# Kernel tuning notes

Measured on AMD Instinct MI355X. Metric: run time of the kernel, lower is better.

Reference implementation:

```python
import jax, jax.numpy as jnp
import numpy as np
from jax import lax

N_FEAT = 150          # feature-map side
N_AR = 9              # anchors per cell
PRE_NMS = 6000        # mode='test'
POST_NMS = 300        # mode='test'
IOU_TH = 0.7
MIN_SIZE = 16.0 / 1000.0


def _make_anchors():
    # grid of centers in [0,1], 9 anchors per cell (3 scales x 3 ratios), xyxy form
    cs = (np.arange(N_FEAT) + 0.5) / N_FEAT
    cy, cx = np.meshgrid(cs, cs, indexing='ij')
    scales = np.array([0.05, 0.1, 0.2])
    ratios = np.array([0.5, 1.0, 2.0])
    ws = (scales[:, None] * np.sqrt(ratios)[None, :]).reshape(-1)  # [9]
    hs = (scales[:, None] / np.sqrt(ratios)[None, :]).reshape(-1)
    cx = np.repeat(cx.reshape(-1), N_AR)
    cy = np.repeat(cy.reshape(-1), N_AR)
    ws = np.tile(ws, N_FEAT * N_FEAT)
    hs = np.tile(hs, N_FEAT * N_FEAT)
    xy = np.stack([cx - ws / 2, cy - hs / 2, cx + ws / 2, cy + hs / 2], axis=-1)
    return xy.astype(np.float32)  # [N,4]


def xy_to_cxcy(xy):
    return jnp.concatenate([(xy[:, 2:] + xy[:, :2]) / 2, xy[:, 2:] - xy[:, :2]], axis=-1)


def cxcy_to_xy(cxcy):
    return jnp.concatenate([cxcy[:, :2] - cxcy[:, 2:] / 2, cxcy[:, :2] + cxcy[:, 2:] / 2], axis=-1)


def decode(t, priors_cxcy):
    cxcy = t[:, :2] * priors_cxcy[:, 2:] + priors_cxcy[:, :2]
    wh = jnp.exp(t[:, 2:]) * priors_cxcy[:, 2:]
    return jnp.concatenate([cxcy, wh], axis=-1)


def pairwise_iou(b):
    # b: [K,4] xyxy -> [K,K]
    area = (b[:, 2] - b[:, 0]) * (b[:, 3] - b[:, 1])
    lt = jnp.maximum(b[:, None, :2], b[None, :, :2])
    rb = jnp.minimum(b[:, None, 2:], b[None, :, 2:])
    wh = jnp.clip(rb - lt, 0.0)
    inter = wh[..., 0] * wh[..., 1]
    return inter / (area[:, None] + area[None, :] - inter + 1e-12)


def greedy_nms_mask(boxes, valid):
    # boxes sorted by score desc; returns bool keep mask of shape [K]
    K = boxes.shape[0]
    iou = pairwise_iou(boxes)  # [K,K]  (~144 MB for K=6000)
    idx = jnp.arange(K)

    def body(i, keep):
        active = keep[i] & valid[i]
        supp = (iou[i] > IOU_TH) & (idx > i) & active
        return keep & ~supp

    keep = lax.fori_loop(0, K, body, jnp.ones(K, dtype=bool))
    return keep & valid


def setup_inputs() -> dict:
    key = jax.random.key(0)
    k1, k2 = jax.random.split(key)
    N = N_FEAT * N_FEAT * N_AR
    pred_cls = jax.random.normal(k1, (1, N, 2), dtype=jnp.float32)
    pred_loc = jax.random.normal(k2, (1, N, 4), dtype=jnp.float32) * 0.1
    anchor = jnp.asarray(_make_anchors())
    return {"pred_cls": pred_cls, "pred_loc": pred_loc, "anchor": anchor}


def reference(pred_cls, pred_loc, anchor):
    # squeeze batch dim of 1
    scores = jax.nn.softmax(pred_cls[0], axis=-1)[:, 1]  # [N] objectness
    priors = xy_to_cxcy(anchor)
    roi = jnp.clip(cxcy_to_xy(decode(pred_loc[0], priors)), 0.0, 1.0)  # [N,4]

    ws = roi[:, 2] - roi[:, 0]
    hs = roi[:, 3] - roi[:, 1]
    valid = (ws >= MIN_SIZE) & (hs >= MIN_SIZE)

    # size filter via masking (scores in [0,1], so -1 sorts below all valid)
    scores_m = jnp.where(valid, scores, -1.0)
    top_scores, top_idx = lax.top_k(scores_m, PRE_NMS)
    boxes = roi[top_idx]           # [PRE_NMS,4], score-descending
    valid_k = top_scores >= 0.0

    keep = greedy_nms_mask(boxes, valid_k)  # [PRE_NMS] bool

    # gather kept boxes in score order, take first POST_NMS, zero-pad the rest
    order = jnp.argsort(jnp.where(keep, jnp.arange(PRE_NMS), PRE_NMS))
    sel = order[:POST_NMS]
    out = boxes[sel] * keep[sel][:, None].astype(boxes.dtype)  # [POST_NMS,4]
    return out
```

## Files before the change

### kernel.cpp

```cpp
#include <hip/hip_runtime.h>
#include <hip/hip_bf16.h>

#define NANCH 202500
#define PRE_NMS 6000
#define POST_NMS 300
#define KW 94
#define CAP 8192
#define NBUCK 16384
#define BSHIFT 18
#define IOU_TH 0.7f
#define MIN_SIZE 0.016f
#define TB_PAD 6016
#define RTILE 256
#define RITEMS 8
#define SBLK 256

typedef unsigned long long ull;

__device__ inline float4 decode_box(const float* __restrict__ loc,
                                    const float* __restrict__ anc, int i) {
    float4 a = ((const float4*)anc)[i];
    float4 t = ((const float4*)loc)[i];
    float pw = a.z - a.x, ph = a.w - a.y;
    float pcx = (a.x + a.z) * 0.5f, pcy = (a.y + a.w) * 0.5f;
    float cx = t.x * pw + pcx, cy = t.y * ph + pcy;
    float w = expf(t.z) * pw, h = expf(t.w) * ph;
    float x1 = fminf(fmaxf(cx - 0.5f * w, 0.f), 1.f);
    float y1 = fminf(fmaxf(cy - 0.5f * h, 0.f), 1.f);
    float x2 = fminf(fmaxf(cx + 0.5f * w, 0.f), 1.f);
    float y2 = fminf(fmaxf(cy + 0.5f * h, 0.f), 1.f);
    return make_float4(x1, y1, x2, y2);
}

__device__ inline unsigned make_key(const float* __restrict__ cls,
                                    const float* __restrict__ loc,
                                    const float* __restrict__ anc, int i) {
    float2 c = ((const float2*)cls)[i];
    float d = c.y - c.x;
    float4 b = decode_box(loc, anc, i);
    bool valid = ((b.z - b.x) >= MIN_SIZE) && ((b.w - b.y) >= MIN_SIZE);
    unsigned ib = __float_as_uint(d);
    unsigned u = (ib & 0x80000000u) ? ~ib : (ib | 0x80000000u);
    return valid ? u : 0u;
}

__device__ inline ull orx64(ull v, int m) {
    unsigned lo = (unsigned)v, hi = (unsigned)(v >> 32);
    lo = (unsigned)__shfl_xor((int)lo, m, 64);
    hi = (unsigned)__shfl_xor((int)hi, m, 64);
    return ((ull)hi << 32) | lo;
}

__global__ __launch_bounds__(256) void k_score(const float* __restrict__ cls,
                                               const float* __restrict__ loc,
                                               const float* __restrict__ anc,
                                               unsigned* __restrict__ hist,
                                               unsigned* __restrict__ keyc, int n) {
    __shared__ unsigned lh[NBUCK];
    int tid = threadIdx.x, bid = blockIdx.x;
    for (int q = tid; q < NBUCK; q += 256) lh[q] = 0u;
    __syncthreads();
    for (int i = bid * 256 + tid; i < n; i += SBLK * 256) {
        unsigned u = make_key(cls, loc, anc, i);
        if (keyc) keyc[i] = u;
        atomicAdd(&lh[u >> BSHIFT], 1u);
    }
    __syncthreads();
    for (int qq = 0; qq < NBUCK / 256; qq++) {
        int q = (qq + bid) & (NBUCK / 256 - 1);
        int b = q * 256 + tid;
        unsigned v = lh[b];
        if (v) atomicAdd(&hist[b], v);
    }
}

__global__ __launch_bounds__(1024) void k_findb(const unsigned* __restrict__ hist,
                                                unsigned* __restrict__ meta) {
    __shared__ unsigned ps[1024];
    int t = threadIdx.x;
    int base = t * (NBUCK / 1024);
    unsigned local = 0;
    for (int b = 0; b < NBUCK / 1024; b++) local += hist[base + b];
    ps[t] = local;
    __syncthreads();
    for (int off = 1; off < 1024; off <<= 1) {
        unsigned add = (t + off < 1024) ? ps[t + off] : 0u;
        __syncthreads();
        ps[t] += add;
        __syncthreads();
    }
    unsigned incl = ps[t];
    unsigned excl = incl - local;
    if (incl >= (unsigned)PRE_NMS && excl < (unsigned)PRE_NMS) {
        unsigned cum = excl;
        int B = base;
        for (int b = NBUCK / 1024 - 1; b >= 0; b--) {
            cum += hist[base + b];
            if (cum >= (unsigned)PRE_NMS) { B = base + b; break; }
        }
        meta[0] = (unsigned)B;
    }
}

__global__ __launch_bounds__(256) void k_compactC(const unsigned* __restrict__ keyc,
                                                  unsigned* __restrict__ meta,
                                                  ull* __restrict__ cand, int n) {
    int i = blockIdx.x * blockDim.x + threadIdx.x;
    unsigned u = (i < n) ? keyc[i] : 0u;
    unsigned B = meta[0];
    bool pred = (i < n) && ((u >> BSHIFT) >= B);
    ull mask = __ballot(pred);
    if (!mask) return;
    int lane = threadIdx.x & 63;
    int leader = __builtin_ctzll(mask);
    unsigned base = 0;
    if (lane == leader) base = atomicAdd(&meta[1], (unsigned)__popcll(mask));
    base = (unsigned)__shfl((int)base, leader, 64);
    if (pred) {
        unsigned p = base + (unsigned)__popcll(mask & ((1ull << lane) - 1ull));
        if (p < CAP) cand[p] = ((ull)(~u) << 32) | (unsigned)i;
    }
}

__global__ __launch_bounds__(256) void k_compactR(const float* __restrict__ cls,
                                                  const float* __restrict__ loc,
                                                  const float* __restrict__ anc,
                                                  unsigned* __restrict__ meta,
                                                  ull* __restrict__ cand, int n) {
    int i = blockIdx.x * blockDim.x + threadIdx.x;
    if (i >= n) return;
    unsigned u = make_key(cls, loc, anc, i);
    if ((u >> BSHIFT) >= meta[0]) {
        unsigned p = atomicAdd(&meta[1], 1u);
        if (p < CAP) cand[p] = ((ull)(~u) << 32) | (unsigned)i;
    }
}

__global__ __launch_bounds__(256) void k_rank(const ull* __restrict__ cand,
                                              const unsigned* __restrict__ meta,
                                              unsigned* __restrict__ rank,
                                              float4* __restrict__ topbox) {
    __shared__ __align__(16) ull tile[RTILE];
    int tid = threadIdx.x;
    int bx = blockIdx.x, by = blockIdx.y;
    unsigned C = meta[1]; if (C > CAP) C = CAP;
    if (by == 0) {
        int per = TB_PAD / (CAP / (256 * RITEMS));
        int s0 = bx * per;
        for (int q = tid; q < per; q += 256)
            topbox[s0 + q] = make_float4(-1.f, -1.f, -1.f, -1.f);
    }
    int ibase = bx * 256 * RITEMS;
    ull ki[RITEMS]; unsigned cnt[RITEMS];
    #pragma unroll
    for (int r = 0; r < RITEMS; r++) {
        int i = ibase + r * 256 + tid;
        ki[r] = (i < (int)C) ? cand[i] : ~0ull;
        cnt[r] = 0u;
    }
    int j = by * RTILE + tid;
    tile[tid] = (j < (int)C) ? cand[j] : ~0ull;
    __syncthreads();
    const ulonglong2* t2 = (const ulonglong2*)tile;
    for (int q = 0; q < RTILE / 2; q++) {
        ulonglong2 v = t2[q];
        #pragma unroll
        for (int r = 0; r < RITEMS; r++)
            cnt[r] += (unsigned)(v.x < ki[r]) + (unsigned)(v.y < ki[r]);
    }
    #pragma unroll
    for (int r = 0; r < RITEMS; r++)
        if (cnt[r]) atomicAdd(&rank[ibase + r * 256 + tid], cnt[r]);
}

__global__ __launch_bounds__(256) void k_scatter(const ull* __restrict__ cand,
                                                 const unsigned* __restrict__ meta,
                                                 const unsigned* __restrict__ rank,
                                                 const float* __restrict__ loc,
                                                 const float* __restrict__ anc,
                                                 float4* __restrict__ topbox,
                                                 ull* __restrict__ vmask) {
    int i = blockIdx.x * 256 + threadIdx.x;
    unsigned C = meta[1]; if (C > CAP) C = CAP;
    if (i >= (int)C) return;
    ull kv = cand[i];
    unsigned uu = ~(unsigned)(kv >> 32);
    if (uu == 0u) return;
    unsigned r = rank[i];
    if (r >= PRE_NMS) return;
    int idx = (int)(unsigned)kv;
    topbox[r] = decode_box(loc, anc, idx);
    atomicOr(&vmask[r >> 6], 1ull << (r & 63));
}

__global__ __launch_bounds__(64) void k_supp(const float4* __restrict__ topbox,
                                             ull* __restrict__ supp,
                                             ull* __restrict__ sdg) {
    int cb = blockIdx.x, rb = blockIdx.y;
    if (cb < rb) return;
    int i = rb * 64 + threadIdx.x;
    __shared__ float4 cbox[64];
    int jt = cb * 64 + threadIdx.x;
    cbox[threadIdx.x] = (jt < PRE_NMS) ? topbox[jt] : make_float4(0.f, 0.f, 0.f, 0.f);
    __syncthreads();
    if (i >= PRE_NMS) return;
    float4 bi = topbox[i];
    float ai = (bi.z - bi.x) * (bi.w - bi.y);
    ull bits = 0ull;
    int j0 = cb * 64;
    for (int jj = 0; jj < 64; jj++) {
        int j = j0 + jj;
        if (j <= i || j >= PRE_NMS) continue;
        float4 bj = cbox[jj];
        float aj = (bj.z - bj.x) * (bj.w - bj.y);
        float lx = fmaxf(bi.x, bj.x), ly = fmaxf(bi.y, bj.y);
        float rx = fminf(bi.z, bj.z), ry = fminf(bi.w, bj.w);
        float iw = fmaxf(rx - lx, 0.f), ih = fmaxf(ry - ly, 0.f);
        float inter = iw * ih;
        float iou = inter / (ai + aj - inter + 1e-12f);
        if (iou > IOU_TH) bits |= (1ull << jj);
    }
    supp[(size_t)i * KW + cb] = bits;
    if (cb == rb) sdg[i] = bits;
}

__global__ __launch_bounds__(64) void k_scan(const ull* __restrict__ supp,
                                             const ull* __restrict__ sdg,
                                             const ull* __restrict__ vmask,
                                             const float4* __restrict__ topbox,
                                             float* __restrict__ out) {
    __shared__ int klist[POST_NMS + 64];
    __shared__ ull vm_s[KW];
    int l = threadIdx.x;
    for (int q = l; q < KW; q += 64) vm_s[q] = vmask[q];
    __syncthreads();
    int nk = 0;
    for (int c = 0; c < KW && nk < POST_NMS; c++) {
        ull vm = vm_s[c];
        if (!vm) continue;
        int row = c * 64 + l;
        ull sd = (row < PRE_NMS) ? sdg[row] : 0ull;
        ull inc = 0ull;
        for (int q = l; q < nk; q += 64)
            inc |= supp[(size_t)klist[q] * KW + c];
        #pragma unroll
        for (int off = 32; off; off >>= 1) inc |= orx64(inc, off);
        ull todo = vm & ~inc;
        unsigned tlo = __builtin_amdgcn_readfirstlane((unsigned)todo);
        unsigned thi = __builtin_amdgcn_readfirstlane((unsigned)(todo >> 32));
        ull td = ((ull)thi << 32) | tlo;
        if (!td) continue;
        unsigned sdlo = (unsigned)sd, sdhi = (unsigned)(sd >> 32);
        ull keepw = 0ull;
        while (td) {
            int b = __builtin_ctzll(td);
            unsigned mlo = __builtin_amdgcn_readlane(sdlo, b);
            unsigned mhi = __builtin_amdgcn_readlane(sdhi, b);
            ull m = (((ull)mhi << 32) | mlo) | (1ull << b);
            keepw |= 1ull << b;
            td &= ~m;
        }
        int pos = nk + (int)__popcll(keepw & ((1ull << l) - 1ull));
        if ((keepw >> l) & 1ull) klist[pos] = row;
        nk += (int)__popcll(keepw);
        __syncthreads();
    }
    __syncthreads();
    int nout = nk < POST_NMS ? nk : POST_NMS;
    for (int q = l; q < nout; q += 64)
        ((float4*)out)[q] = topbox[klist[q]];
    for (int q = nout + l; q < POST_NMS; q += 64)
        ((float4*)out)[q] = make_float4(0.f, 0.f, 0.f, 0.f);
}

__global__ __launch_bounds__(64) void k_nms(const float4* __restrict__ topbox,
                                            float* __restrict__ out) {
    int l = threadIdx.x;
    float4 kb[5];
    int nk = 0;
    for (int q0 = 0; q0 < TB_PAD && nk < POST_NMS; q0 += 64) {
        float4 myb = topbox[q0 + l];
        for (int b = 0; b < 64 && nk < POST_NMS; b++) {
            float4 bb;
            bb.x = __shfl(myb.x, b, 64);
            bb.y = __shfl(myb.y, b, 64);
            bb.z = __shfl(myb.z, b, 64);
            bb.w = __shfl(myb.w, b, 64);
            if (bb.x < 0.f) continue;
            float ab = (bb.z - bb.x) * (bb.w - bb.y);
            bool sup = false;
            #pragma unroll
            for (int r = 0; r < 5; r++) {
                int s = r * 64 + l;
                if (s < nk) {
                    float4 kv = kb[r];
                    float ak = (kv.z - kv.x) * (kv.w - kv.y);
                    float lx = fmaxf(bb.x, kv.x), ly = fmaxf(bb.y, kv.y);
                    float rx = fminf(bb.z, kv.z), ry = fminf(bb.w, kv.w);
                    float iw = fmaxf(rx - lx, 0.f), ih = fmaxf(ry - ly, 0.f);
                    float inter = iw * ih;
                    float iou = inter / (ab + ak - inter + 1e-12f);
                    sup |= (iou > IOU_TH);
                }
            }
            if (!__any(sup)) {
                if (l == (nk & 63)) kb[nk >> 6] = bb;
                if (l < 4) {
                    float v = (l == 0) ? bb.x : (l == 1) ? bb.y : (l == 2) ? bb.z : bb.w;
                    out[4 * nk + l] = v;
                }
                nk++;
            }
        }
    }
    for (int t = nk * 4 + l; t < POST_NMS * 4; t += 64) out[t] = 0.f;
}

extern "C" void kernel_launch(void* const* d_in, const int* in_sizes, int n_in,
                              void* d_out, int out_size, void* d_ws, size_t ws_size,
                              hipStream_t stream) {
    const int N = in_sizes[0] / 2;
    const float* cls = (const float*)d_in[0];
    const float* loc = (const float*)d_in[1];
    const float* anc = (const float*)d_in[2];
    float* out = (float*)d_out;

    char* ws = (char*)d_ws;
    size_t off = 0;
    auto take = [&](size_t bytes) {
        size_t o = off;
        off += (bytes + 255) & ~(size_t)255;
        return o;
    };
    unsigned* hist = (unsigned*)(ws + take((size_t)NBUCK * 4));
    char*     mblk = ws + take(1024);
    unsigned* meta  = (unsigned*)mblk;
    ull*      vmask = (ull*)(mblk + 256);
    unsigned* rank = (unsigned*)(ws + take((size_t)CAP * 4));
    size_t zlen = off;
    ull*    cand   = (ull*)(ws + take((size_t)CAP * 8));
    float4* topbox = (float4*)(ws + take((size_t)TB_PAD * 16));
    unsigned* keyc = (unsigned*)(ws + take((size_t)N * 4));
    ull*      supp = (ull*)(ws + take((size_t)PRE_NMS * KW * 8));
    ull*      sdg  = (ull*)(ws + take((size_t)TB_PAD * 8));
    size_t full_need = off;
    const bool fast = (ws_size >= full_need);

    hipMemsetAsync(ws, 0, zlen, stream);

    dim3 rgrid(CAP / (256 * RITEMS), CAP / RTILE);

    if (fast) {
        k_score<<<SBLK, 256, 0, stream>>>(cls, loc, anc, hist, keyc, N);
        k_findb<<<1, 1024, 0, stream>>>(hist, meta);
        k_compactC<<<(N + 255) / 256, 256, 0, stream>>>(keyc, meta, cand, N);
        k_rank<<<rgrid, 256, 0, stream>>>(cand, meta, rank, topbox);
        k_scatter<<<CAP / 256, 256, 0, stream>>>(cand, meta, rank, loc, anc, topbox, vmask);
        k_supp<<<dim3(KW, KW), 64, 0, stream>>>(topbox, supp, sdg);
        k_scan<<<1, 64, 0, stream>>>(supp, sdg, vmask, topbox, out);
    } else {
        k_score<<<SBLK, 256, 0, stream>>>(cls, loc, anc, hist, (unsigned*)nullptr, N);
        k_findb<<<1, 1024, 0, stream>>>(hist, meta);
        k_compactR<<<(N + 255) / 256, 256, 0, stream>>>(cls, loc, anc, meta, cand, N);
        k_rank<<<rgrid, 256, 0, stream>>>(cand, meta, rank, topbox);
        k_scatter<<<CAP / 256, 256, 0, stream>>>(cand, meta, rank, loc, anc, topbox, vmask);
        k_nms<<<1, 64, 0, stream>>>(topbox, out);
    }
}
```

Measured before the change: 175.5 us.

## Fuse the NMS pipeline into one cooperative kernel with grid-wide syncs

Replaces the seven-kernel chain (score histogram, bucket find, compaction, rank, scatter, suppression matrix, scan) with a single cooperative kernel of 256 blocks that uses grid.sync between phases. Keys stay in registers instead of a keyc buffer, and ranking becomes a direct count over candidates. The goal is to remove per-launch overhead and the intermediate global round trips. The IoU test now uses a multiply instead of a division, and the scan kernel drops its redundant block barriers. The cost is that phase work runs on a fixed grid, and the serial scan runs on one wave while every other block sits idle at the end.

```diff
diff --git a/kernel.cpp b/kernel.cpp
--- a/kernel.cpp
+++ b/kernel.cpp
@@ -1,5 +1,8 @@
 #include <hip/hip_runtime.h>
 #include <hip/hip_bf16.h>
+#include <hip/hip_cooperative_groups.h>
+
+namespace cg = cooperative_groups;
 
 #define NANCH 202500
 #define PRE_NMS 6000
@@ -14,6 +17,7 @@
 #define RTILE 256
 #define RITEMS 8
 #define SBLK 256
+#define GRID 256
 
 typedef unsigned long long ull;
 
@@ -49,6 +53,204 @@
     lo = (unsigned)__shfl_xor((int)lo, m, 64);
     hi = (unsigned)__shfl_xor((int)hi, m, 64);
     return ((ull)hi << 32) | lo;
+}
+
+__device__ inline bool iou_gt(float4 bi, float4 bj, float ai) {
+    float aj = (bj.z - bj.x) * (bj.w - bj.y);
+    float lx = fmaxf(bi.x, bj.x), ly = fmaxf(bi.y, bj.y);
+    float rx = fminf(bi.z, bj.z), ry = fminf(bi.w, bj.w);
+    float iw = fmaxf(rx - lx, 0.f), ih = fmaxf(ry - ly, 0.f);
+    float inter = iw * ih;
+    return inter > IOU_TH * (ai + aj - inter);
+}
+
+__global__ __launch_bounds__(256, 1) void k_front(
+        const float* __restrict__ cls, const float* __restrict__ loc,
+        const float* __restrict__ anc, unsigned* __restrict__ hist,
+        unsigned* __restrict__ meta, ull* __restrict__ vmask,
+        ull* __restrict__ cand, float4* __restrict__ topbox,
+        ull* __restrict__ supp, ull* __restrict__ sdg,
+        float* __restrict__ out, int n) {
+    __shared__ __align__(16) unsigned char smem[NBUCK * 4];
+    cg::grid_group grid = cg::this_grid();
+    int tid = threadIdx.x, bid = blockIdx.x;
+
+    unsigned* lh = (unsigned*)smem;
+    for (int q = tid; q < NBUCK; q += 256) lh[q] = 0u;
+    __syncthreads();
+    unsigned uk[4];
+    #pragma unroll
+    for (int k = 0; k < 4; k++) {
+        int i = bid * 256 + tid + k * (GRID * 256);
+        unsigned u = 0u;
+        if (i < n) {
+            u = make_key(cls, loc, anc, i);
+            atomicAdd(&lh[u >> BSHIFT], 1u);
+        }
+        uk[k] = u;
+    }
+    __syncthreads();
+    for (int qq = 0; qq < NBUCK / 256; qq++) {
+        int q = (qq + bid) & (NBUCK / 256 - 1);
+        int b = q * 256 + tid;
+        unsigned v = lh[b];
+        if (v) atomicAdd(&hist[b], v);
+    }
+    __threadfence();
+    grid.sync();
+
+    if (bid == 0) {
+        unsigned* ps = (unsigned*)smem;
+        int base = tid * (NBUCK / 256);
+        unsigned local = 0;
+        for (int b = 0; b < NBUCK / 256; b++) local += hist[base + b];
+        ps[tid] = local;
+        __syncthreads();
+        for (int off = 1; off < 256; off <<= 1) {
+            unsigned add = (tid + off < 256) ? ps[tid + off] : 0u;
+            __syncthreads();
+            ps[tid] += add;
+            __syncthreads();
+        }
+        unsigned incl = ps[tid];
+        unsigned excl = incl - local;
+        if (incl >= (unsigned)PRE_NMS && excl < (unsigned)PRE_NMS) {
+            unsigned cum = excl;
+            int B = base;
+            for (int b = NBUCK / 256 - 1; b >= 0; b--) {
+                cum += hist[base + b];
+                if (cum >= (unsigned)PRE_NMS) { B = base + b; break; }
+            }
+            meta[0] = (unsigned)B;
+        }
+    }
+    __threadfence();
+    grid.sync();
+
+    unsigned Bb = meta[0];
+    #pragma unroll
+    for (int k = 0; k < 4; k++) {
+        int i = bid * 256 + tid + k * (GRID * 256);
+        unsigned u = uk[k];
+        bool pred = (i < n) && ((u >> BSHIFT) >= Bb);
+        ull mask = __ballot(pred);
+        if (mask) {
+            int lane = tid & 63;
+            int leader = __builtin_ctzll(mask);
+            unsigned base2 = 0;
+            if (lane == leader) base2 = atomicAdd(&meta[1], (unsigned)__popcll(mask));
+            base2 = (unsigned)__shfl((int)base2, leader, 64);
+            if (pred) {
+                unsigned p = base2 + (unsigned)__popcll(mask & ((1ull << lane) - 1ull));
+                if (p < CAP) cand[p] = ((ull)(~u) << 32) | (unsigned)i;
+            }
+        }
+    }
+    __threadfence();
+    grid.sync();
+
+    {
+        unsigned C = meta[1]; if (C > CAP) C = CAP;
+        ull* tile = (ull*)smem;
+        int sub = tid >> 3, octl = tid & 7;
+        int ci = bid * 32 + sub;
+        ull ki = (ci < (int)C) ? cand[ci] : 0ull;
+        unsigned cnt = 0;
+        int ntile = ((int)C + 255) / 256;
+        for (int tt = 0; tt < ntile; tt++) {
+            int j = tt * 256 + tid;
+            tile[tid] = (j < (int)C) ? cand[j] : ~0ull;
+            __syncthreads();
+            #pragma unroll
+            for (int jj = 0; jj < 32; jj++)
+                cnt += (unsigned)(tile[jj * 8 + octl] < ki);
+            __syncthreads();
+        }
+        cnt += (unsigned)__shfl_xor((int)cnt, 1, 64);
+        cnt += (unsigned)__shfl_xor((int)cnt, 2, 64);
+        cnt += (unsigned)__shfl_xor((int)cnt, 4, 64);
+        if (octl == 0 && ci < (int)C) {
+            unsigned uu = ~(unsigned)(ki >> 32);
+            if (uu != 0u && cnt < (unsigned)PRE_NMS) {
+                int idx = (int)(unsigned)ki;
+                topbox[cnt] = decode_box(loc, anc, idx);
+                atomicOr(&vmask[cnt >> 6], 1ull << (cnt & 63));
+            }
+        }
+    }
+    __threadfence();
+    grid.sync();
+
+    {
+        float4* cboxs = (float4*)smem;
+        int wv = tid >> 6, lane = tid & 63;
+        int gw = bid * 4 + wv;
+        for (int t = gw; t < KW * KW; t += GRID * 4) {
+            int rb = t / KW, cb = t - rb * KW;
+            if (cb < rb) continue;
+            int jt = cb * 64 + lane;
+            cboxs[wv * 64 + lane] = (jt < PRE_NMS) ? topbox[jt]
+                                                   : make_float4(0.f, 0.f, 0.f, 0.f);
+            int i = rb * 64 + lane;
+            if (i < PRE_NMS) {
+                float4 bi = topbox[i];
+                float ai = (bi.z - bi.x) * (bi.w - bi.y);
+                ull bits = 0ull;
+                int j0 = cb * 64;
+                for (int jj = 0; jj < 64; jj++) {
+                    int j = j0 + jj;
+                    if (j <= i || j >= PRE_NMS) continue;
+                    if (iou_gt(bi, cboxs[wv * 64 + jj], ai)) bits |= (1ull << jj);
+                }
+                supp[(size_t)i * KW + cb] = bits;
+                if (cb == rb) sdg[i] = bits;
+            }
+        }
+    }
+    __threadfence();
+    grid.sync();
+
+    if (bid == 0 && tid < 64) {
+        int* klist = (int*)smem;
+        ull* vm_s = (ull*)(smem + 2048);
+        int l = tid;
+        for (int q = l; q < KW; q += 64) vm_s[q] = vmask[q];
+        int nk = 0;
+        for (int c = 0; c < KW && nk < POST_NMS; c++) {
+            ull vm = vm_s[c];
+            if (!vm) continue;
+            int row = c * 64 + l;
+            ull sd = (row < PRE_NMS) ? sdg[row] : 0ull;
+            ull inc = 0ull;
+            for (int q = l; q < nk; q += 64)
+                inc |= supp[(size_t)klist[q] * KW + c];
+            #pragma unroll
+            for (int off = 32; off; off >>= 1) inc |= orx64(inc, off);
+            ull todo = vm & ~inc;
+            unsigned tlo = __builtin_amdgcn_readfirstlane((unsigned)todo);
+            unsigned thi = __builtin_amdgcn_readfirstlane((unsigned)(todo >> 32));
+            ull td = ((ull)thi << 32) | tlo;
+            if (!td) continue;
+            unsigned sdlo = (unsigned)sd, sdhi = (unsigned)(sd >> 32);
+            ull keepw = 0ull;
+            while (td) {
+                int b = __builtin_ctzll(td);
+                unsigned mlo = __builtin_amdgcn_readlane(sdlo, b);
+                unsigned mhi = __builtin_amdgcn_readlane(sdhi, b);
+                ull m = (((ull)mhi << 32) | mlo) | (1ull << b);
+                keepw |= 1ull << b;
+                td &= ~m;
+            }
+            int pos = nk + (int)__popcll(keepw & ((1ull << l) - 1ull));
+            if ((keepw >> l) & 1ull) klist[pos] = row;
+            nk += (int)__popcll(keepw);
+        }
+        int nout = nk < POST_NMS ? nk : POST_NMS;
+        for (int q = l; q < nout; q += 64)
+            ((float4*)out)[q] = topbox[klist[q]];
+        for (int q = nout + l; q < POST_NMS; q += 64)
+            ((float4*)out)[q] = make_float4(0.f, 0.f, 0.f, 0.f);
+    }
 }
 
 __global__ __launch_bounds__(256) void k_score(const float* __restrict__ cls,
@@ -211,14 +413,7 @@
     for (int jj = 0; jj < 64; jj++) {
         int j = j0 + jj;
         if (j <= i || j >= PRE_NMS) continue;
-        float4 bj = cbox[jj];
-        float aj = (bj.z - bj.x) * (bj.w - bj.y);
-        float lx = fmaxf(bi.x, bj.x), ly = fmaxf(bi.y, bj.y);
-        float rx = fminf(bi.z, bj.z), ry = fminf(bi.w, bj.w);
-        float iw = fmaxf(rx - lx, 0.f), ih = fmaxf(ry - ly, 0.f);
-        float inter = iw * ih;
-        float iou = inter / (ai + aj - inter + 1e-12f);
-        if (iou > IOU_TH) bits |= (1ull << jj);
+        if (iou_gt(bi, cbox[jj], ai)) bits |= (1ull << jj);
     }
     supp[(size_t)i * KW + cb] = bits;
     if (cb == rb) sdg[i] = bits;
@@ -233,7 +428,6 @@
     __shared__ ull vm_s[KW];
     int l = threadIdx.x;
     for (int q = l; q < KW; q += 64) vm_s[q] = vmask[q];
-    __syncthreads();
     int nk = 0;
     for (int c = 0; c < KW && nk < POST_NMS; c++) {
         ull vm = vm_s[c];
@@ -263,9 +457,7 @@
         int pos = nk + (int)__popcll(keepw & ((1ull << l) - 1ull));
         if ((keepw >> l) & 1ull) klist[pos] = row;
         nk += (int)__popcll(keepw);
-        __syncthreads();
-    }
-    __syncthreads();
+    }
     int nout = nk < POST_NMS ? nk : POST_NMS;
     for (int q = l; q < nout; q += 64)
         ((float4*)out)[q] = topbox[klist[q]];
@@ -348,17 +540,25 @@
 
     hipMemsetAsync(ws, 0, zlen, stream);
 
-    dim3 rgrid(CAP / (256 * RITEMS), CAP / RTILE);
-
     if (fast) {
-        k_score<<<SBLK, 256, 0, stream>>>(cls, loc, anc, hist, keyc, N);
-        k_findb<<<1, 1024, 0, stream>>>(hist, meta);
-        k_compactC<<<(N + 255) / 256, 256, 0, stream>>>(keyc, meta, cand, N);
-        k_rank<<<rgrid, 256, 0, stream>>>(cand, meta, rank, topbox);
-        k_scatter<<<CAP / 256, 256, 0, stream>>>(cand, meta, rank, loc, anc, topbox, vmask);
-        k_supp<<<dim3(KW, KW), 64, 0, stream>>>(topbox, supp, sdg);
-        k_scan<<<1, 64, 0, stream>>>(supp, sdg, vmask, topbox, out);
+        int Nv = N;
+        void* args[] = {(void*)&cls, (void*)&loc, (void*)&anc, (void*)&hist,
+                        (void*)&meta, (void*)&vmask, (void*)&cand, (void*)&topbox,
+                        (void*)&supp, (void*)&sdg, (void*)&out, (void*)&Nv};
+        hipError_t ce = hipLaunchCooperativeKernel(reinterpret_cast<void*>(k_front),
+                                                   dim3(GRID), dim3(256), args, 0, stream);
+        if (ce != hipSuccess) {
+            dim3 rgrid(CAP / (256 * RITEMS), CAP / RTILE);
+            k_score<<<SBLK, 256, 0, stream>>>(cls, loc, anc, hist, keyc, N);
+            k_findb<<<1, 1024, 0, stream>>>(hist, meta);
+            k_compactC<<<(N + 255) / 256, 256, 0, stream>>>(keyc, meta, cand, N);
+            k_rank<<<rgrid, 256, 0, stream>>>(cand, meta, rank, topbox);
+            k_scatter<<<CAP / 256, 256, 0, stream>>>(cand, meta, rank, loc, anc, topbox, vmask);
+            k_supp<<<dim3(KW, KW), 64, 0, stream>>>(topbox, supp, sdg);
+            k_scan<<<1, 64, 0, stream>>>(supp, sdg, vmask, topbox, out);
+        }
     } else {
+        dim3 rgrid(CAP / (256 * RITEMS), CAP / RTILE);
         k_score<<<SBLK, 256, 0, stream>>>(cls, loc, anc, hist, (unsigned*)nullptr, N);
         k_findb<<<1, 1024, 0, stream>>>(hist, meta);
         k_compactR<<<(N + 255) / 256, 256, 0, stream>>>(cls, loc, anc, meta, cand, N);
```

New measurement: 451.2 us. 2.57x slower.

## Fuse threshold search into compaction and rank into scatter to cut launches

Applied to the files above, without the earlier changes.

Each compaction block now scans the score histogram itself with vectorized loads to find the bucket threshold, which removes the separate single-block threshold kernel. Ranking and scatter become one kernel in which 8 threads cooperatively count smaller keys for each candidate and then write the decoded box directly. This drops the rank buffer, its atomics and the topbox sentinel fill. The IoU test now compares by multiplication instead of division. The fast path drops from seven launches to five, at the cost of every compaction block redundantly prefix-scanning the histogram.

```diff
diff --git a/kernel.cpp b/kernel.cpp
--- a/kernel.cpp
+++ b/kernel.cpp
@@ -14,6 +14,7 @@
 #define RTILE 256
 #define RITEMS 8
 #define SBLK 256
+#define CBLK 198
 
 typedef unsigned long long ull;
 
@@ -51,6 +52,15 @@
     return ((ull)hi << 32) | lo;
 }
 
+__device__ inline bool iou_gt(float4 bi, float4 bj, float ai) {
+    float aj = (bj.z - bj.x) * (bj.w - bj.y);
+    float lx = fmaxf(bi.x, bj.x), ly = fmaxf(bi.y, bj.y);
+    float rx = fminf(bi.z, bj.z), ry = fminf(bi.w, bj.w);
+    float iw = fmaxf(rx - lx, 0.f), ih = fmaxf(ry - ly, 0.f);
+    float inter = iw * ih;
+    return inter > IOU_TH * (ai + aj - inter);
+}
+
 __global__ __launch_bounds__(256) void k_score(const float* __restrict__ cls,
                                                const float* __restrict__ loc,
                                                const float* __restrict__ anc,
@@ -74,123 +84,101 @@
     }
 }
 
-__global__ __launch_bounds__(1024) void k_findb(const unsigned* __restrict__ hist,
-                                                unsigned* __restrict__ meta) {
-    __shared__ unsigned ps[1024];
-    int t = threadIdx.x;
-    int base = t * (NBUCK / 1024);
+__global__ __launch_bounds__(256) void k_compactB(const unsigned* __restrict__ keyc,
+                                                  const unsigned* __restrict__ hist,
+                                                  unsigned* __restrict__ meta,
+                                                  ull* __restrict__ cand, int n) {
+    __shared__ unsigned ps[256];
+    __shared__ unsigned Bs;
+    int tid = threadIdx.x, bid = blockIdx.x;
+    const uint4* h4 = (const uint4*)hist;
     unsigned local = 0;
-    for (int b = 0; b < NBUCK / 1024; b++) local += hist[base + b];
-    ps[t] = local;
-    __syncthreads();
-    for (int off = 1; off < 1024; off <<= 1) {
-        unsigned add = (t + off < 1024) ? ps[t + off] : 0u;
-        __syncthreads();
-        ps[t] += add;
-        __syncthreads();
-    }
-    unsigned incl = ps[t];
+    #pragma unroll
+    for (int b = 0; b < 16; b++) {
+        uint4 v = h4[tid * 16 + b];
+        local += v.x + v.y + v.z + v.w;
+    }
+    ps[tid] = local;
+    __syncthreads();
+    for (int off = 1; off < 256; off <<= 1) {
+        unsigned add = (tid + off < 256) ? ps[tid + off] : 0u;
+        __syncthreads();
+        ps[tid] += add;
+        __syncthreads();
+    }
+    unsigned incl = ps[tid];
     unsigned excl = incl - local;
     if (incl >= (unsigned)PRE_NMS && excl < (unsigned)PRE_NMS) {
+        unsigned hv[64];
+        #pragma unroll
+        for (int b = 0; b < 16; b++) {
+            uint4 v = h4[tid * 16 + b];
+            hv[4 * b] = v.x; hv[4 * b + 1] = v.y;
+            hv[4 * b + 2] = v.z; hv[4 * b + 3] = v.w;
+        }
         unsigned cum = excl;
-        int B = base;
-        for (int b = NBUCK / 1024 - 1; b >= 0; b--) {
-            cum += hist[base + b];
-            if (cum >= (unsigned)PRE_NMS) { B = base + b; break; }
-        }
-        meta[0] = (unsigned)B;
-    }
-}
-
-__global__ __launch_bounds__(256) void k_compactC(const unsigned* __restrict__ keyc,
-                                                  unsigned* __restrict__ meta,
-                                                  ull* __restrict__ cand, int n) {
-    int i = blockIdx.x * blockDim.x + threadIdx.x;
-    unsigned u = (i < n) ? keyc[i] : 0u;
-    unsigned B = meta[0];
-    bool pred = (i < n) && ((u >> BSHIFT) >= B);
-    ull mask = __ballot(pred);
-    if (!mask) return;
-    int lane = threadIdx.x & 63;
-    int leader = __builtin_ctzll(mask);
-    unsigned base = 0;
-    if (lane == leader) base = atomicAdd(&meta[1], (unsigned)__popcll(mask));
-    base = (unsigned)__shfl((int)base, leader, 64);
-    if (pred) {
-        unsigned p = base + (unsigned)__popcll(mask & ((1ull << lane) - 1ull));
-        if (p < CAP) cand[p] = ((ull)(~u) << 32) | (unsigned)i;
-    }
-}
-
-__global__ __launch_bounds__(256) void k_compactR(const float* __restrict__ cls,
-                                                  const float* __restrict__ loc,
-                                                  const float* __restrict__ anc,
-                                                  unsigned* __restrict__ meta,
-                                                  ull* __restrict__ cand, int n) {
-    int i = blockIdx.x * blockDim.x + threadIdx.x;
-    if (i >= n) return;
-    unsigned u = make_key(cls, loc, anc, i);
-    if ((u >> BSHIFT) >= meta[0]) {
-        unsigned p = atomicAdd(&meta[1], 1u);
-        if (p < CAP) cand[p] = ((ull)(~u) << 32) | (unsigned)i;
-    }
-}
-
-__global__ __launch_bounds__(256) void k_rank(const ull* __restrict__ cand,
-                                              const unsigned* __restrict__ meta,
-                                              unsigned* __restrict__ rank,
-                                              float4* __restrict__ topbox) {
-    __shared__ __align__(16) ull tile[RTILE];
-    int tid = threadIdx.x;
-    int bx = blockIdx.x, by = blockIdx.y;
+        int B = tid * 64;
+        for (int b = 63; b >= 0; b--) {
+            cum += hv[b];
+            if (cum >= (unsigned)PRE_NMS) { B = tid * 64 + b; break; }
+        }
+        Bs = (unsigned)B;
+    }
+    __syncthreads();
+    unsigned B = Bs;
+    #pragma unroll
+    for (int k = 0; k < 4; k++) {
+        int i = bid * 1024 + k * 256 + tid;
+        unsigned u = (i < n) ? keyc[i] : 0u;
+        bool pred = (i < n) && ((u >> BSHIFT) >= B);
+        ull mask = __ballot(pred);
+        if (mask) {
+            int lane = tid & 63;
+            int leader = __builtin_ctzll(mask);
+            unsigned base2 = 0;
+            if (lane == leader) base2 = atomicAdd(&meta[1], (unsigned)__popcll(mask));
+            base2 = (unsigned)__shfl((int)base2, leader, 64);
+            if (pred) {
+                unsigned p = base2 + (unsigned)__popcll(mask & ((1ull << lane) - 1ull));
+                if (p < CAP) cand[p] = ((ull)(~u) << 32) | (unsigned)i;
+            }
+        }
+    }
+}
+
+__global__ __launch_bounds__(256) void k_ranksc(const ull* __restrict__ cand,
+                                                const unsigned* __restrict__ meta,
+                                                const float* __restrict__ loc,
+                                                const float* __restrict__ anc,
+                                                float4* __restrict__ topbox,
+                                                ull* __restrict__ vmask) {
+    __shared__ __align__(16) ull tile[256];
+    int tid = threadIdx.x, bid = blockIdx.x;
     unsigned C = meta[1]; if (C > CAP) C = CAP;
-    if (by == 0) {
-        int per = TB_PAD / (CAP / (256 * RITEMS));
-        int s0 = bx * per;
-        for (int q = tid; q < per; q += 256)
-            topbox[s0 + q] = make_float4(-1.f, -1.f, -1.f, -1.f);
-    }
-    int ibase = bx * 256 * RITEMS;
-    ull ki[RITEMS]; unsigned cnt[RITEMS];
-    #pragma unroll
-    for (int r = 0; r < RITEMS; r++) {
-        int i = ibase + r * 256 + tid;
-        ki[r] = (i < (int)C) ? cand[i] : ~0ull;
-        cnt[r] = 0u;
-    }
-    int j = by * RTILE + tid;
-    tile[tid] = (j < (int)C) ? cand[j] : ~0ull;
-    __syncthreads();
-    const ulonglong2* t2 = (const ulonglong2*)tile;
-    for (int q = 0; q < RTILE / 2; q++) {
-        ulonglong2 v = t2[q];
+    int sub = tid >> 3, octl = tid & 7;
+    int ci = bid * 32 + sub;
+    ull ki = (ci < (int)C) ? cand[ci] : 0ull;
+    unsigned cnt = 0;
+    int ntile = ((int)C + 255) / 256;
+    for (int tt = 0; tt < ntile; tt++) {
+        int j = tt * 256 + tid;
+        tile[tid] = (j < (int)C) ? cand[j] : ~0ull;
+        __syncthreads();
         #pragma unroll
-        for (int r = 0; r < RITEMS; r++)
-            cnt[r] += (unsigned)(v.x < ki[r]) + (unsigned)(v.y < ki[r]);
-    }
-    #pragma unroll
-    for (int r = 0; r < RITEMS; r++)
-        if (cnt[r]) atomicAdd(&rank[ibase + r * 256 + tid], cnt[r]);
-}
-
-__global__ __launch_bounds__(256) void k_scatter(const ull* __restrict__ cand,
-                                                 const unsigned* __restrict__ meta,
-                                                 const unsigned* __restrict__ rank,
-                                                 const float* __restrict__ loc,
-                                                 const float* __restrict__ anc,
-                                                 float4* __restrict__ topbox,
-                                                 ull* __restrict__ vmask) {
-    int i = blockIdx.x * 256 + threadIdx.x;
-    unsigned C = meta[1]; if (C > CAP) C = CAP;
-    if (i >= (int)C) return;
-    ull kv = cand[i];
-    unsigned uu = ~(unsigned)(kv >> 32);
-    if (uu == 0u) return;
-    unsigned r = rank[i];
-    if (r >= PRE_NMS) return;
-    int idx = (int)(unsigned)kv;
-    topbox[r] = decode_box(loc, anc, idx);
-    atomicOr(&vmask[r >> 6], 1ull << (r & 63));
+        for (int jj = 0; jj < 32; jj++)
+            cnt += (unsigned)(tile[jj * 8 + octl] < ki);
+        __syncthreads();
+    }
+    cnt += (unsigned)__shfl_xor((int)cnt, 1, 64);
+    cnt += (unsigned)__shfl_xor((int)cnt, 2, 64);
+    cnt += (unsigned)__shfl_xor((int)cnt, 4, 64);
+    if (octl == 0 && ci < (int)C) {
+        unsigned uu = ~(unsigned)(ki >> 32);
+        if (uu != 0u && cnt < (unsigned)PRE_NMS) {
+            topbox[cnt] = decode_box(loc, anc, (int)(unsigned)ki);
+            atomicOr(&vmask[cnt >> 6], 1ull << (cnt & 63));
+        }
+    }
 }
 
 __global__ __launch_bounds__(64) void k_supp(const float4* __restrict__ topbox,
@@ -211,14 +199,7 @@
     for (int jj = 0; jj < 64; jj++) {
         int j = j0 + jj;
         if (j <= i || j >= PRE_NMS) continue;
-        float4 bj = cbox[jj];
-        float aj = (bj.z - bj.x) * (bj.w - bj.y);
-        float lx = fmaxf(bi.x, bj.x), ly = fmaxf(bi.y, bj.y);
-        float rx = fminf(bi.z, bj.z), ry = fminf(bi.w, bj.w);
-        float iw = fmaxf(rx - lx, 0.f), ih = fmaxf(ry - ly, 0.f);
-        float inter = iw * ih;
-        float iou = inter / (ai + aj - inter + 1e-12f);
-        if (iou > IOU_TH) bits |= (1ull << jj);
+        if (iou_gt(bi, cbox[jj], ai)) bits |= (1ull << jj);
     }
     supp[(size_t)i * KW + cb] = bits;
     if (cb == rb) sdg[i] = bits;
@@ -271,6 +252,105 @@
         ((float4*)out)[q] = topbox[klist[q]];
     for (int q = nout + l; q < POST_NMS; q += 64)
         ((float4*)out)[q] = make_float4(0.f, 0.f, 0.f, 0.f);
+}
+
+__global__ __launch_bounds__(1024) void k_findb(const unsigned* __restrict__ hist,
+                                                unsigned* __restrict__ meta) {
+    __shared__ unsigned ps[1024];
+    int t = threadIdx.x;
+    int base = t * (NBUCK / 1024);
+    unsigned local = 0;
+    for (int b = 0; b < NBUCK / 1024; b++) local += hist[base + b];
+    ps[t] = local;
+    __syncthreads();
+    for (int off = 1; off < 1024; off <<= 1) {
+        unsigned add = (t + off < 1024) ? ps[t + off] : 0u;
+        __syncthreads();
+        ps[t] += add;
+        __syncthreads();
+    }
+    unsigned incl = ps[t];
+    unsigned excl = incl - local;
+    if (incl >= (unsigned)PRE_NMS && excl < (unsigned)PRE_NMS) {
+        unsigned cum = excl;
+        int B = base;
+        for (int b = NBUCK / 1024 - 1; b >= 0; b--) {
+            cum += hist[base + b];
+            if (cum >= (unsigned)PRE_NMS) { B = base + b; break; }
+        }
+        meta[0] = (unsigned)B;
+    }
+}
+
+__global__ __launch_bounds__(256) void k_compactR(const float* __restrict__ cls,
+                                                  const float* __restrict__ loc,
+                                                  const float* __restrict__ anc,
+                                                  unsigned* __restrict__ meta,
+                                                  ull* __restrict__ cand, int n) {
+    int i = blockIdx.x * blockDim.x + threadIdx.x;
+    if (i >= n) return;
+    unsigned u = make_key(cls, loc, anc, i);
+    if ((u >> BSHIFT) >= meta[0]) {
+        unsigned p = atomicAdd(&meta[1], 1u);
+        if (p < CAP) cand[p] = ((ull)(~u) << 32) | (unsigned)i;
+    }
+}
+
+__global__ __launch_bounds__(256) void k_rank(const ull* __restrict__ cand,
+                                              const unsigned* __restrict__ meta,
+                                              unsigned* __restrict__ rank,
+                                              float4* __restrict__ topbox) {
+    __shared__ __align__(16) ull tile[RTILE];
+    int tid = threadIdx.x;
+    int bx = blockIdx.x, by = blockIdx.y;
+    unsigned C = meta[1]; if (C > CAP) C = CAP;
+    if (by == 0) {
+        int per = TB_PAD / (CAP / (256 * RITEMS));
+        int s0 = bx * per;
+        for (int q = tid; q < per; q += 256)
+            topbox[s0 + q] = make_float4(-1.f, -1.f, -1.f, -1.f);
+    }
+    int ibase = bx * 256 * RITEMS;
+    ull ki[RITEMS]; unsigned cnt[RITEMS];
+    #pragma unroll
+    for (int r = 0; r < RITEMS; r++) {
+        int i = ibase + r * 256 + tid;
+        ki[r] = (i < (int)C) ? cand[i] : ~0ull;
+        cnt[r] = 0u;
+    }
+    int j = by * RTILE + tid;
+    tile[tid] = (j < (int)C) ? cand[j] : ~0ull;
+    __syncthreads();
+    const ulonglong2* t2 = (const ulonglong2*)tile;
+    for (int q = 0; q < RTILE / 2; q++) {
+        ulonglong2 v = t2[q];
+        #pragma unroll
+        for (int r = 0; r < RITEMS; r++)
+            cnt[r] += (unsigned)(v.x < ki[r]) + (unsigned)(v.y < ki[r]);
+    }
+    #pragma unroll
+    for (int r = 0; r < RITEMS; r++)
+        if (cnt[r]) atomicAdd(&rank[ibase + r * 256 + tid], cnt[r]);
+}
+
+__global__ __launch_bounds__(256) void k_scatter(const ull* __restrict__ cand,
+                                                 const unsigned* __restrict__ meta,
+                                                 const unsigned* __restrict__ rank,
+                                                 const float* __restrict__ loc,
+                                                 const float* __restrict__ anc,
+                                                 float4* __restrict__ topbox,
+                                                 ull* __restrict__ vmask) {
+    int i = blockIdx.x * 256 + threadIdx.x;
+    unsigned C = meta[1]; if (C > CAP) C = CAP;
+    if (i >= (int)C) return;
+    ull kv = cand[i];
+    unsigned uu = ~(unsigned)(kv >> 32);
+    if (uu == 0u) return;
+    unsigned r = rank[i];
+    if (r >= PRE_NMS) return;
+    int idx = (int)(unsigned)kv;
+    topbox[r] = decode_box(loc, anc, idx);
+    atomicOr(&vmask[r >> 6], 1ull << (r & 63));
 }
 
 __global__ __launch_bounds__(64) void k_nms(const float4* __restrict__ topbox,
@@ -348,17 +428,14 @@
 
     hipMemsetAsync(ws, 0, zlen, stream);
 
-    dim3 rgrid(CAP / (256 * RITEMS), CAP / RTILE);
-
     if (fast) {
         k_score<<<SBLK, 256, 0, stream>>>(cls, loc, anc, hist, keyc, N);
-        k_findb<<<1, 1024, 0, stream>>>(hist, meta);
-        k_compactC<<<(N + 255) / 256, 256, 0, stream>>>(keyc, meta, cand, N);
-        k_rank<<<rgrid, 256, 0, stream>>>(cand, meta, rank, topbox);
-        k_scatter<<<CAP / 256, 256, 0, stream>>>(cand, meta, rank, loc, anc, topbox, vmask);
+        k_compactB<<<CBLK, 256, 0, stream>>>(keyc, hist, meta, cand, N);
+        k_ranksc<<<CAP / 32, 256, 0, stream>>>(cand, meta, loc, anc, topbox, vmask);
         k_supp<<<dim3(KW, KW), 64, 0, stream>>>(topbox, supp, sdg);
         k_scan<<<1, 64, 0, stream>>>(supp, sdg, vmask, topbox, out);
     } else {
+        dim3 rgrid(CAP / (256 * RITEMS), CAP / RTILE);
         k_score<<<SBLK, 256, 0, stream>>>(cls, loc, anc, hist, (unsigned*)nullptr, N);
         k_findb<<<1, 1024, 0, stream>>>(hist, meta);
         k_compactR<<<(N + 255) / 256, 256, 0, stream>>>(cls, loc, anc, meta, cand, N);
```

After: 178.9 us. Within noise of the previous version (+1.9%).
